# Performance work log

Hardware: AMD Instinct MI355X
Metric: run time of the kernel (lower is better)

The kernel has to match this reference:

```python
import jax, jax.numpy as jnp
import numpy as np

B, S, E = 4, 2048, 512
Q, FFN = 8, 2048


def setup_inputs() -> dict:
    key = jax.random.key(0)
    k_x, k_th, k_w1, k_w2 = jax.random.split(key, 4)
    x = jax.random.normal(k_x, (B, S, E), dtype=jnp.float32)
    # trainable RY angles, one per wire
    theta = jax.random.normal(k_th, (Q,), dtype=jnp.float32)
    W1 = jax.random.normal(k_w1, (Q, FFN), dtype=jnp.float32) / np.sqrt(Q)
    b1 = jnp.zeros((FFN,), dtype=jnp.float32)
    W2 = jax.random.normal(k_w2, (FFN, E), dtype=jnp.float32) / np.sqrt(FFN)
    b2 = jnp.zeros((E,), dtype=jnp.float32)
    return {"x": x, "theta": theta, "W1": W1, "b1": b1, "W2": W2, "b2": b2}


def reference(x, theta, W1, b1, W2, b2):
    # Quantum circuit: |0> -> RX(x_i) -> RY(theta_i) -> <Z> per wire.
    # No entangling gates, so the 8-qubit state factorizes; simulate each
    # qubit's 2 complex amplitudes, batched over all tokens & wires at once.
    n_wires = theta.shape[0]
    xq = x[..., :n_wires]                     # encoder uses input_idx 0..7: [B,S,Q]
    # RX(x)|0> = cos(x/2)|0> - i sin(x/2)|1>
    a = jnp.cos(xq * 0.5).astype(jnp.complex64)
    b = (-1j) * jnp.sin(xq * 0.5).astype(jnp.complex64)
    # RY(theta) = [[c,-s],[s,c]], c=cos(theta/2), s=sin(theta/2)
    c = jnp.cos(theta * 0.5).astype(jnp.complex64)
    s = jnp.sin(theta * 0.5).astype(jnp.complex64)
    a2 = c * a - s * b
    b2_ = s * a + c * b
    # <Z> = |amp0|^2 - |amp1|^2  -> [B,S,Q]
    z = (jnp.abs(a2) ** 2 - jnp.abs(b2_) ** 2).astype(x.dtype)
    # dropout is identity at inference
    h = jax.nn.relu(jnp.einsum('bsq,qf->bsf', z, W1) + b1)
    return jnp.einsum('bsf,fe->bse', h, W2) + b2
```

## Files before the change

### kernel.cpp

```cpp
#include <hip/hip_runtime.h>
#include <hip/hip_bf16.h>

typedef __bf16 bf16_t;
typedef __bf16 bf16x4 __attribute__((ext_vector_type(4)));
typedef __bf16 bf16x8 __attribute__((ext_vector_type(8)));
typedef float f32x4 __attribute__((ext_vector_type(4)));

#define M_TOT 8192
#define N_TOT 512
#define K_TOT 2048
#define E_TOT 512
#define NSEG_HALF 8

__device__ __forceinline__ bf16x8 zero8() {
    bf16x8 v;
#pragma unroll
    for (int i = 0; i < 8; ++i) v[i] = (bf16_t)0.0f;
    return v;
}

__global__ __launch_bounds__(256)
void prep4_kernel(const float* __restrict__ x,
                  const float* __restrict__ theta,
                  const float* __restrict__ W1,
                  const float* __restrict__ b1,
                  const float* __restrict__ W2,
                  bf16_t* __restrict__ W2t,
                  bf16_t* __restrict__ zb,
                  bf16_t* __restrict__ W1p)
{
    const int b = blockIdx.x;
    if (b < 256) {
        __shared__ bf16_t T[64][66];
        const int k0 = (b >> 3) * 64;
        const int n0 = (b & 7) * 64;
        const int kl = threadIdx.x >> 4;
        const int n4 = threadIdx.x & 15;
#pragma unroll
        for (int i = 0; i < 4; ++i) {
            int k = kl + i * 16;
            float4 v = *(const float4*)(W2 + (size_t)(k0 + k) * N_TOT + n0 + n4 * 4);
            T[n4 * 4 + 0][k] = (bf16_t)v.x;
            T[n4 * 4 + 1][k] = (bf16_t)v.y;
            T[n4 * 4 + 2][k] = (bf16_t)v.z;
            T[n4 * 4 + 3][k] = (bf16_t)v.w;
        }
        __syncthreads();
        const int nl = threadIdx.x >> 4;
        const int k4 = threadIdx.x & 15;
#pragma unroll
        for (int i = 0; i < 4; ++i) {
            int n = nl + i * 16;
            bf16x4 v;
            v[0] = T[n][k4 * 4 + 0];
            v[1] = T[n][k4 * 4 + 1];
            v[2] = T[n][k4 * 4 + 2];
            v[3] = T[n][k4 * 4 + 3];
            *(bf16x4*)(W2t + (size_t)(n0 + n) * K_TOT + k0 + k4 * 4) = v;
        }
    } else if (b < 288) {
        const int m = (b - 256) * 256 + threadIdx.x;
        float4 x0 = *(const float4*)(x + (size_t)m * E_TOT);
        float4 x1 = *(const float4*)(x + (size_t)m * E_TOT + 4);
        float xs[8] = {x0.x, x0.y, x0.z, x0.w, x1.x, x1.y, x1.z, x1.w};
        bf16x8 lo;
#pragma unroll
        for (int q = 0; q < 8; ++q)
            lo[q] = (bf16_t)(__builtin_cosf(theta[q]) * __builtin_cosf(xs[q]));
        bf16x8 hi = zero8();
        hi[0] = (bf16_t)1.0f;
        *(bf16x8*)(zb + (size_t)m * 16)     = lo;
        *(bf16x8*)(zb + (size_t)m * 16 + 8) = hi;
    } else {
        const int d  = (b - 288) * 256 + threadIdx.x;
        const int c  = d >> 5;
        const int dd = d & 31;
        const int p  = dd >> 4;
        const int rr = dd & 15;
        const int f  = c * 32 + ((rr >> 2) << 3) + (p << 2) + (rr & 3);
        bf16x8 lo;
#pragma unroll
        for (int q = 0; q < 8; ++q)
            lo[q] = (bf16_t)W1[(size_t)q * K_TOT + f];
        bf16x8 hi = zero8();
        hi[0] = (bf16_t)b1[f];
        *(bf16x8*)(W1p + (size_t)d * 16)     = lo;
        *(bf16x8*)(W1p + (size_t)d * 16 + 8) = hi;
    }
}

__device__ __forceinline__ void stage_B(const bf16_t* __restrict__ W2t,
                                        bf16_t* dst_buf, int n_base, int k0,
                                        int wl, int l) {
#pragma unroll
    for (int j = 0; j < 4; ++j) {
        int s    = wl * 64 + l + j * 256;
        int tile = s >> 9;
        int n    = (s >> 3) & 63;
        int g    = (s & 7) ^ (n & 7);
        const bf16_t* src = W2t + (size_t)(n_base + n) * K_TOT
                            + k0 + tile * 64 + g * 8;
        bf16_t* ldst = dst_buf + (size_t)(wl * 64 + j * 256) * 8;
        __builtin_amdgcn_global_load_lds(
            (const __attribute__((address_space(1))) unsigned int*)src,
            (__attribute__((address_space(3))) unsigned int*)ldst,
            16, 0, 0);
    }
}

__device__ __forceinline__ void load_wf(const bf16_t* __restrict__ W1p, int k0,
                                        int l15, int lq, bf16x8 wf[4]) {
#pragma unroll
    for (int i = 0; i < 4; ++i) wf[i] = zero8();
    if (lq < 2) {
        const int base = (k0 >> 5) * 2;
#pragma unroll
        for (int i = 0; i < 4; ++i)
            wf[i] = *(const bf16x8*)(W1p + (size_t)((base + i) * 16 + l15) * 16 + lq * 8);
    }
}

__device__ __forceinline__ void compute_tile(const bf16_t* Bb, const bf16x8 wf[4],
                                             const bf16x8 zfrag[2],
                                             int l15, int lq,
                                             f32x4 acc[2][4]) {
    bf16x8 bfr[2][4];
#pragma unroll
    for (int c = 0; c < 2; ++c)
#pragma unroll
        for (int nt = 0; nt < 4; ++nt) {
            int r = nt * 16 + l15;
            int s = (c * 4 + lq) ^ (r & 7);
            bfr[c][nt] = *(const bf16x8*)(Bb + r * 64 + s * 8);
        }

    bf16x8 af[2][2];
#pragma unroll
    for (int mt = 0; mt < 2; ++mt)
#pragma unroll
        for (int c = 0; c < 2; ++c) {
            f32x4 h0 = (f32x4){0.f, 0.f, 0.f, 0.f};
            f32x4 h1 = (f32x4){0.f, 0.f, 0.f, 0.f};
            h0 = __builtin_amdgcn_mfma_f32_16x16x32_bf16(wf[c * 2 + 0], zfrag[mt], h0, 0, 0, 0);
            h1 = __builtin_amdgcn_mfma_f32_16x16x32_bf16(wf[c * 2 + 1], zfrag[mt], h1, 0, 0, 0);
            bf16x8 a;
#pragma unroll
            for (int r = 0; r < 4; ++r) {
                a[r]     = (bf16_t)fmaxf(h0[r], 0.f);
                a[r + 4] = (bf16_t)fmaxf(h1[r], 0.f);
            }
            af[mt][c] = a;
        }

#pragma unroll
    for (int c = 0; c < 2; ++c)
#pragma unroll
        for (int mt = 0; mt < 2; ++mt)
#pragma unroll
            for (int nt = 0; nt < 4; ++nt)
                acc[mt][nt] = __builtin_amdgcn_mfma_f32_16x16x32_bf16(
                    af[mt][c], bfr[c][nt], acc[mt][nt], 0, 0, 0);
}

__global__ __launch_bounds__(512, 4)
void ffq_gemm_kernel(const bf16_t* __restrict__ zb,
                     const bf16_t* __restrict__ W1p,
                     const bf16_t* __restrict__ W2t,
                     const float* __restrict__ b2,
                     float* __restrict__ out)
{
    __shared__ bf16_t Blds[2][2][2 * 64 * 64];

    const int t  = threadIdx.x;
    const int w  = t >> 6, l = t & 63;
    const int ks = w >> 2;
    const int wl = w & 3;
    const int m_base = blockIdx.y * 128;
    const int n_base = blockIdx.x * 64;
    const int l15 = l & 15, lq = l >> 4;
    const int k_base = ks * 1024;

    bf16x8 zfrag[2];
#pragma unroll
    for (int mt = 0; mt < 2; ++mt) {
        zfrag[mt] = zero8();
        if (lq < 2)
            zfrag[mt] = *(const bf16x8*)(zb + (size_t)(m_base + wl * 32 + mt * 16 + l15) * 16 + lq * 8);
    }

    f32x4 acc[2][4];
#pragma unroll
    for (int mt = 0; mt < 2; ++mt)
#pragma unroll
        for (int nt = 0; nt < 4; ++nt)
            acc[mt][nt] = (f32x4){0.f, 0.f, 0.f, 0.f};

    stage_B(W2t, Blds[ks][0], n_base, k_base, wl, l);

    for (int s = 0; s < NSEG_HALF; ++s) {
        const int cur = s & 1;
        __syncthreads();
        if (s + 1 < NSEG_HALF)
            stage_B(W2t, Blds[ks][1 - cur], n_base, k_base + (s + 1) * 128, wl, l);

#pragma unroll
        for (int tt = 0; tt < 2; ++tt) {
            bf16x8 wf[4];
            load_wf(W1p, k_base + s * 128 + tt * 64, l15, lq, wf);
            compute_tile(Blds[ks][cur] + tt * 4096, wf, zfrag, l15, lq, acc);
        }
    }

    __syncthreads();
    float* F = (float*)&Blds[0][0][0];
    if (ks == 1) {
#pragma unroll
        for (int mt = 0; mt < 2; ++mt)
#pragma unroll
            for (int nt = 0; nt < 4; ++nt) {
                int idx = ((wl * 2 + mt) * 4 + nt) * 64 + l;
                *(f32x4*)(F + (size_t)idx * 4) = acc[mt][nt];
            }
    }
    __syncthreads();
    if (ks == 0) {
#pragma unroll
        for (int nt = 0; nt < 4; ++nt) {
            int col = n_base + nt * 16 + l15;
            float bias = b2[col];
#pragma unroll
            for (int mt = 0; mt < 2; ++mt) {
                int idx = ((wl * 2 + mt) * 4 + nt) * 64 + l;
                f32x4 part = *(const f32x4*)(F + (size_t)idx * 4);
#pragma unroll
                for (int r = 0; r < 4; ++r) {
                    int row = m_base + wl * 32 + mt * 16 + lq * 4 + r;
                    out[(size_t)row * N_TOT + col] = acc[mt][nt][r] + part[r] + bias;
                }
            }
        }
    }
}

extern "C" void kernel_launch(void* const* d_in, const int* in_sizes, int n_in,
                              void* d_out, int out_size, void* d_ws, size_t ws_size,
                              hipStream_t stream) {
    const float* x     = (const float*)d_in[0];
    const float* theta = (const float*)d_in[1];
    const float* W1    = (const float*)d_in[2];
    const float* b1    = (const float*)d_in[3];
    const float* W2    = (const float*)d_in[4];
    const float* b2    = (const float*)d_in[5];
    float* out = (float*)d_out;

    const size_t W2T_BYTES = (size_t)N_TOT * K_TOT * sizeof(bf16_t);
    const size_t ZB_BYTES  = (size_t)M_TOT * 16 * sizeof(bf16_t);

    bf16_t* W2t = (bf16_t*)d_ws;
    bf16_t* zb  = (bf16_t*)((char*)d_ws + W2T_BYTES);
    bf16_t* W1p = (bf16_t*)((char*)d_ws + W2T_BYTES + ZB_BYTES);

    prep4_kernel<<<296, 256, 0, stream>>>(x, theta, W1, b1, W2, W2t, zb, W1p);

    dim3 grid(N_TOT / 64, M_TOT / 128);
    ffq_gemm_kernel<<<grid, 512, 0, stream>>>(zb, W1p, W2t, b2, out);
}
```

Measured before the change: 103.2 us.

## Fuse prep and GEMM kernels into one cooperative kernel with grid sync

Merges the preprocessing stage (W2 transpose to bf16, z feature computation, W1 packing) and the fused two-layer GEMM into a single cooperative launch of 512 blocks. The stages are separated by a grid-wide barrier. The aim is to remove the second kernel launch and the gap between the dependent kernels. The trade-off is the cost of a grid-wide barrier and the need for all blocks to be co-resident; if the cooperative launch fails, the code falls back to the original two-kernel path.

```diff
diff --git a/kernel.cpp b/kernel.cpp
--- a/kernel.cpp
+++ b/kernel.cpp
@@ -1,5 +1,8 @@
 #include <hip/hip_runtime.h>
+#include <hip/hip_cooperative_groups.h>
 #include <hip/hip_bf16.h>
+
+namespace cg = cooperative_groups;
 
 typedef __bf16 bf16_t;
 typedef __bf16 bf16x4 __attribute__((ext_vector_type(4)));
@@ -17,6 +20,237 @@
 #pragma unroll
     for (int i = 0; i < 8; ++i) v[i] = (bf16_t)0.0f;
     return v;
+}
+
+__device__ __forceinline__ void stage_B(const bf16_t* __restrict__ W2t,
+                                        bf16_t* dst_buf, int n_base, int k0,
+                                        int wl, int l) {
+#pragma unroll
+    for (int j = 0; j < 4; ++j) {
+        int s    = wl * 64 + l + j * 256;
+        int tile = s >> 9;
+        int n    = (s >> 3) & 63;
+        int g    = (s & 7) ^ (n & 7);
+        const bf16_t* src = W2t + (size_t)(n_base + n) * K_TOT
+                            + k0 + tile * 64 + g * 8;
+        bf16_t* ldst = dst_buf + (size_t)(wl * 64 + j * 256) * 8;
+        __builtin_amdgcn_global_load_lds(
+            (const __attribute__((address_space(1))) unsigned int*)src,
+            (__attribute__((address_space(3))) unsigned int*)ldst,
+            16, 0, 0);
+    }
+}
+
+__device__ __forceinline__ void load_wf(const bf16_t* __restrict__ W1p, int k0,
+                                        int l15, int lq, bf16x8 wf[4]) {
+#pragma unroll
+    for (int i = 0; i < 4; ++i) wf[i] = zero8();
+    if (lq < 2) {
+        const int base = (k0 >> 5) * 2;
+#pragma unroll
+        for (int i = 0; i < 4; ++i)
+            wf[i] = *(const bf16x8*)(W1p + (size_t)((base + i) * 16 + l15) * 16 + lq * 8);
+    }
+}
+
+__device__ __forceinline__ void compute_tile(const bf16_t* Bb, const bf16x8 wf[4],
+                                             const bf16x8 zfrag[2],
+                                             int l15, int lq,
+                                             f32x4 acc[2][4]) {
+    bf16x8 bfr[2][4];
+#pragma unroll
+    for (int c = 0; c < 2; ++c)
+#pragma unroll
+        for (int nt = 0; nt < 4; ++nt) {
+            int r = nt * 16 + l15;
+            int s = (c * 4 + lq) ^ (r & 7);
+            bfr[c][nt] = *(const bf16x8*)(Bb + r * 64 + s * 8);
+        }
+
+    bf16x8 af[2][2];
+#pragma unroll
+    for (int mt = 0; mt < 2; ++mt)
+#pragma unroll
+        for (int c = 0; c < 2; ++c) {
+            f32x4 h0 = (f32x4){0.f, 0.f, 0.f, 0.f};
+            f32x4 h1 = (f32x4){0.f, 0.f, 0.f, 0.f};
+            h0 = __builtin_amdgcn_mfma_f32_16x16x32_bf16(wf[c * 2 + 0], zfrag[mt], h0, 0, 0, 0);
+            h1 = __builtin_amdgcn_mfma_f32_16x16x32_bf16(wf[c * 2 + 1], zfrag[mt], h1, 0, 0, 0);
+            bf16x8 a;
+#pragma unroll
+            for (int r = 0; r < 4; ++r) {
+                a[r]     = (bf16_t)fmaxf(h0[r], 0.f);
+                a[r + 4] = (bf16_t)fmaxf(h1[r], 0.f);
+            }
+            af[mt][c] = a;
+        }
+
+#pragma unroll
+    for (int c = 0; c < 2; ++c)
+#pragma unroll
+        for (int mt = 0; mt < 2; ++mt)
+#pragma unroll
+            for (int nt = 0; nt < 4; ++nt)
+                acc[mt][nt] = __builtin_amdgcn_mfma_f32_16x16x32_bf16(
+                    af[mt][c], bfr[c][nt], acc[mt][nt], 0, 0, 0);
+}
+
+__device__ __forceinline__ void gemm_body(int b_n, int b_m, int t,
+                                          const bf16_t* __restrict__ zb,
+                                          const bf16_t* __restrict__ W1p,
+                                          const bf16_t* __restrict__ W2t,
+                                          const float* __restrict__ b2,
+                                          float* __restrict__ out,
+                                          bf16_t (*Blds)[2][2 * 64 * 64]) {
+    const int w  = t >> 6, l = t & 63;
+    const int ks = w >> 2;
+    const int wl = w & 3;
+    const int m_base = b_m * 128;
+    const int n_base = b_n * 64;
+    const int l15 = l & 15, lq = l >> 4;
+    const int k_base = ks * 1024;
+
+    bf16x8 zfrag[2];
+#pragma unroll
+    for (int mt = 0; mt < 2; ++mt) {
+        zfrag[mt] = zero8();
+        if (lq < 2)
+            zfrag[mt] = *(const bf16x8*)(zb + (size_t)(m_base + wl * 32 + mt * 16 + l15) * 16 + lq * 8);
+    }
+
+    f32x4 acc[2][4];
+#pragma unroll
+    for (int mt = 0; mt < 2; ++mt)
+#pragma unroll
+        for (int nt = 0; nt < 4; ++nt)
+            acc[mt][nt] = (f32x4){0.f, 0.f, 0.f, 0.f};
+
+    stage_B(W2t, Blds[ks][0], n_base, k_base, wl, l);
+
+    for (int s = 0; s < NSEG_HALF; ++s) {
+        const int cur = s & 1;
+        __syncthreads();
+        if (s + 1 < NSEG_HALF)
+            stage_B(W2t, Blds[ks][1 - cur], n_base, k_base + (s + 1) * 128, wl, l);
+
+#pragma unroll
+        for (int tt = 0; tt < 2; ++tt) {
+            bf16x8 wf[4];
+            load_wf(W1p, k_base + s * 128 + tt * 64, l15, lq, wf);
+            compute_tile(Blds[ks][cur] + tt * 4096, wf, zfrag, l15, lq, acc);
+        }
+    }
+
+    __syncthreads();
+    float* F = (float*)&Blds[0][0][0];
+    if (ks == 1) {
+#pragma unroll
+        for (int mt = 0; mt < 2; ++mt)
+#pragma unroll
+            for (int nt = 0; nt < 4; ++nt) {
+                int idx = ((wl * 2 + mt) * 4 + nt) * 64 + l;
+                *(f32x4*)(F + (size_t)idx * 4) = acc[mt][nt];
+            }
+    }
+    __syncthreads();
+    if (ks == 0) {
+#pragma unroll
+        for (int nt = 0; nt < 4; ++nt) {
+            int col = n_base + nt * 16 + l15;
+            float bias = b2[col];
+#pragma unroll
+            for (int mt = 0; mt < 2; ++mt) {
+                int idx = ((wl * 2 + mt) * 4 + nt) * 64 + l;
+                f32x4 part = *(const f32x4*)(F + (size_t)idx * 4);
+#pragma unroll
+                for (int r = 0; r < 4; ++r) {
+                    int row = m_base + wl * 32 + mt * 16 + lq * 4 + r;
+                    out[(size_t)row * N_TOT + col] = acc[mt][nt][r] + part[r] + bias;
+                }
+            }
+        }
+    }
+}
+
+__global__ __launch_bounds__(512, 4)
+void ffq_fused_kernel(const float* __restrict__ x,
+                      const float* __restrict__ theta,
+                      const float* __restrict__ W1,
+                      const float* __restrict__ b1,
+                      const float* __restrict__ W2,
+                      const float* __restrict__ b2,
+                      bf16_t* __restrict__ W2t,
+                      bf16_t* __restrict__ zb,
+                      bf16_t* __restrict__ W1p,
+                      float* __restrict__ out)
+{
+    __shared__ bf16_t Blds[2][2][2 * 64 * 64];
+
+    const int b = blockIdx.x;
+    const int t = threadIdx.x;
+
+    if (b < 256) {
+        bf16_t (*T)[66] = reinterpret_cast<bf16_t (*)[66]>(&Blds[0][0][0]);
+        const int k0 = (b >> 3) * 64;
+        const int n0 = (b & 7) * 64;
+        const int kl = t >> 4;
+        const int n4 = t & 15;
+#pragma unroll
+        for (int i = 0; i < 2; ++i) {
+            int k = kl + i * 32;
+            float4 v = *(const float4*)(W2 + (size_t)(k0 + k) * N_TOT + n0 + n4 * 4);
+            T[n4 * 4 + 0][k] = (bf16_t)v.x;
+            T[n4 * 4 + 1][k] = (bf16_t)v.y;
+            T[n4 * 4 + 2][k] = (bf16_t)v.z;
+            T[n4 * 4 + 3][k] = (bf16_t)v.w;
+        }
+        __syncthreads();
+        const int nl = t >> 4;
+        const int k4 = t & 15;
+#pragma unroll
+        for (int i = 0; i < 2; ++i) {
+            int n = nl + i * 32;
+            bf16x4 v;
+            v[0] = T[n][k4 * 4 + 0];
+            v[1] = T[n][k4 * 4 + 1];
+            v[2] = T[n][k4 * 4 + 2];
+            v[3] = T[n][k4 * 4 + 3];
+            *(bf16x4*)(W2t + (size_t)(n0 + n) * K_TOT + k0 + k4 * 4) = v;
+        }
+    } else if (b < 272) {
+        const int m = (b - 256) * 512 + t;
+        float4 x0 = *(const float4*)(x + (size_t)m * E_TOT);
+        float4 x1 = *(const float4*)(x + (size_t)m * E_TOT + 4);
+        float xs[8] = {x0.x, x0.y, x0.z, x0.w, x1.x, x1.y, x1.z, x1.w};
+        bf16x8 lo;
+#pragma unroll
+        for (int q = 0; q < 8; ++q)
+            lo[q] = (bf16_t)(__builtin_cosf(theta[q]) * __builtin_cosf(xs[q]));
+        bf16x8 hi = zero8();
+        hi[0] = (bf16_t)1.0f;
+        *(bf16x8*)(zb + (size_t)m * 16)     = lo;
+        *(bf16x8*)(zb + (size_t)m * 16 + 8) = hi;
+    } else if (b < 276) {
+        const int d  = (b - 272) * 512 + t;
+        const int c  = d >> 5;
+        const int dd = d & 31;
+        const int p  = dd >> 4;
+        const int rr = dd & 15;
+        const int f  = c * 32 + ((rr >> 2) << 3) + (p << 2) + (rr & 3);
+        bf16x8 lo;
+#pragma unroll
+        for (int q = 0; q < 8; ++q)
+            lo[q] = (bf16_t)W1[(size_t)q * K_TOT + f];
+        bf16x8 hi = zero8();
+        hi[0] = (bf16_t)b1[f];
+        *(bf16x8*)(W1p + (size_t)d * 16)     = lo;
+        *(bf16x8*)(W1p + (size_t)d * 16 + 8) = hi;
+    }
+
+    __threadfence();
+    cg::this_grid().sync();
+
+    gemm_body(b & 7, b >> 3, t, zb, W1p, W2t, b2, out, Blds);
 }
 
 __global__ __launch_bounds__(256)
@@ -89,79 +323,6 @@
     }
 }
 
-__device__ __forceinline__ void stage_B(const bf16_t* __restrict__ W2t,
-                                        bf16_t* dst_buf, int n_base, int k0,
-                                        int wl, int l) {
-#pragma unroll
-    for (int j = 0; j < 4; ++j) {
-        int s    = wl * 64 + l + j * 256;
-        int tile = s >> 9;
-        int n    = (s >> 3) & 63;
-        int g    = (s & 7) ^ (n & 7);
-        const bf16_t* src = W2t + (size_t)(n_base + n) * K_TOT
-                            + k0 + tile * 64 + g * 8;
-        bf16_t* ldst = dst_buf + (size_t)(wl * 64 + j * 256) * 8;
-        __builtin_amdgcn_global_load_lds(
-            (const __attribute__((address_space(1))) unsigned int*)src,
-            (__attribute__((address_space(3))) unsigned int*)ldst,
-            16, 0, 0);
-    }
-}
-
-__device__ __forceinline__ void load_wf(const bf16_t* __restrict__ W1p, int k0,
-                                        int l15, int lq, bf16x8 wf[4]) {
-#pragma unroll
-    for (int i = 0; i < 4; ++i) wf[i] = zero8();
-    if (lq < 2) {
-        const int base = (k0 >> 5) * 2;
-#pragma unroll
-        for (int i = 0; i < 4; ++i)
-            wf[i] = *(const bf16x8*)(W1p + (size_t)((base + i) * 16 + l15) * 16 + lq * 8);
-    }
-}
-
-__device__ __forceinline__ void compute_tile(const bf16_t* Bb, const bf16x8 wf[4],
-                                             const bf16x8 zfrag[2],
-                                             int l15, int lq,
-                                             f32x4 acc[2][4]) {
-    bf16x8 bfr[2][4];
-#pragma unroll
-    for (int c = 0; c < 2; ++c)
-#pragma unroll
-        for (int nt = 0; nt < 4; ++nt) {
-            int r = nt * 16 + l15;
-            int s = (c * 4 + lq) ^ (r & 7);
-            bfr[c][nt] = *(const bf16x8*)(Bb + r * 64 + s * 8);
-        }
-
-    bf16x8 af[2][2];
-#pragma unroll
-    for (int mt = 0; mt < 2; ++mt)
-#pragma unroll
-        for (int c = 0; c < 2; ++c) {
-            f32x4 h0 = (f32x4){0.f, 0.f, 0.f, 0.f};
-            f32x4 h1 = (f32x4){0.f, 0.f, 0.f, 0.f};
-            h0 = __builtin_amdgcn_mfma_f32_16x16x32_bf16(wf[c * 2 + 0], zfrag[mt], h0, 0, 0, 0);
-            h1 = __builtin_amdgcn_mfma_f32_16x16x32_bf16(wf[c * 2 + 1], zfrag[mt], h1, 0, 0, 0);
-            bf16x8 a;
-#pragma unroll
-            for (int r = 0; r < 4; ++r) {
-                a[r]     = (bf16_t)fmaxf(h0[r], 0.f);
-                a[r + 4] = (bf16_t)fmaxf(h1[r], 0.f);
-            }
-            af[mt][c] = a;
-        }
-
-#pragma unroll
-    for (int c = 0; c < 2; ++c)
-#pragma unroll
-        for (int mt = 0; mt < 2; ++mt)
-#pragma unroll
-            for (int nt = 0; nt < 4; ++nt)
-                acc[mt][nt] = __builtin_amdgcn_mfma_f32_16x16x32_bf16(
-                    af[mt][c], bfr[c][nt], acc[mt][nt], 0, 0, 0);
-}
-
 __global__ __launch_bounds__(512, 4)
 void ffq_gemm_kernel(const bf16_t* __restrict__ zb,
                      const bf16_t* __restrict__ W1p,
@@ -170,76 +331,7 @@
                      float* __restrict__ out)
 {
     __shared__ bf16_t Blds[2][2][2 * 64 * 64];
-
-    const int t  = threadIdx.x;
-    const int w  = t >> 6, l = t & 63;
-    const int ks = w >> 2;
-    const int wl = w & 3;
-    const int m_base = blockIdx.y * 128;
-    const int n_base = blockIdx.x * 64;
-    const int l15 = l & 15, lq = l >> 4;
-    const int k_base = ks * 1024;
-
-    bf16x8 zfrag[2];
-#pragma unroll
-    for (int mt = 0; mt < 2; ++mt) {
-        zfrag[mt] = zero8();
-        if (lq < 2)
-            zfrag[mt] = *(const bf16x8*)(zb + (size_t)(m_base + wl * 32 + mt * 16 + l15) * 16 + lq * 8);
-    }
-
-    f32x4 acc[2][4];
-#pragma unroll
-    for (int mt = 0; mt < 2; ++mt)
-#pragma unroll
-        for (int nt = 0; nt < 4; ++nt)
-            acc[mt][nt] = (f32x4){0.f, 0.f, 0.f, 0.f};
-
-    stage_B(W2t, Blds[ks][0], n_base, k_base, wl, l);
-
-    for (int s = 0; s < NSEG_HALF; ++s) {
-        const int cur = s & 1;
-        __syncthreads();
-        if (s + 1 < NSEG_HALF)
-            stage_B(W2t, Blds[ks][1 - cur], n_base, k_base + (s + 1) * 128, wl, l);
-
-#pragma unroll
-        for (int tt = 0; tt < 2; ++tt) {
-            bf16x8 wf[4];
-            load_wf(W1p, k_base + s * 128 + tt * 64, l15, lq, wf);
-            compute_tile(Blds[ks][cur] + tt * 4096, wf, zfrag, l15, lq, acc);
-        }
-    }
-
-    __syncthreads();
-    float* F = (float*)&Blds[0][0][0];
-    if (ks == 1) {
-#pragma unroll
-        for (int mt = 0; mt < 2; ++mt)
-#pragma unroll
-            for (int nt = 0; nt < 4; ++nt) {
-                int idx = ((wl * 2 + mt) * 4 + nt) * 64 + l;
-                *(f32x4*)(F + (size_t)idx * 4) = acc[mt][nt];
-            }
-    }
-    __syncthreads();
-    if (ks == 0) {
-#pragma unroll
-        for (int nt = 0; nt < 4; ++nt) {
-            int col = n_base + nt * 16 + l15;
-            float bias = b2[col];
-#pragma unroll
-            for (int mt = 0; mt < 2; ++mt) {
-                int idx = ((wl * 2 + mt) * 4 + nt) * 64 + l;
-                f32x4 part = *(const f32x4*)(F + (size_t)idx * 4);
-#pragma unroll
-                for (int r = 0; r < 4; ++r) {
-                    int row = m_base + wl * 32 + mt * 16 + lq * 4 + r;
-                    out[(size_t)row * N_TOT + col] = acc[mt][nt][r] + part[r] + bias;
-                }
-            }
-        }
-    }
+    gemm_body(blockIdx.x, blockIdx.y, threadIdx.x, zb, W1p, W2t, b2, out, Blds);
 }
 
 extern "C" void kernel_launch(void* const* d_in, const int* in_sizes, int n_in,
@@ -260,8 +352,16 @@
     bf16_t* zb  = (bf16_t*)((char*)d_ws + W2T_BYTES);
     bf16_t* W1p = (bf16_t*)((char*)d_ws + W2T_BYTES + ZB_BYTES);
 
-    prep4_kernel<<<296, 256, 0, stream>>>(x, theta, W1, b1, W2, W2t, zb, W1p);
-
-    dim3 grid(N_TOT / 64, M_TOT / 128);
-    ffq_gemm_kernel<<<grid, 512, 0, stream>>>(zb, W1p, W2t, b2, out);
-}
+    void* args[] = { (void*)&x, (void*)&theta, (void*)&W1, (void*)&b1,
+                     (void*)&W2, (void*)&b2, (void*)&W2t, (void*)&zb,
+                     (void*)&W1p, (void*)&out };
+    hipError_t err = hipLaunchCooperativeKernel(
+        reinterpret_cast<void*>(ffq_fused_kernel),
+        dim3(512), dim3(512), args, 0, stream);
+
+    if (err != hipSuccess) {
+        prep4_kernel<<<296, 256, 0, stream>>>(x, theta, W1, b1, W2, W2t, zb, W1p);
+        dim3 grid(N_TOT / 64, M_TOT / 128);
+        ffq_gemm_kernel<<<grid, 512, 0, stream>>>(zb, W1p, W2t, b2, out);
+    }
+}
```

Result: slower. 263.1 us (+155.0%).
